# Kernel tuning notes

Measured on AMD Instinct MI355X. Metric: run time of the kernel, lower is better.

The kernel has to match this reference:

```python
import jax, jax.numpy as jnp
import numpy as np

RADIUS = 0.22
NB = 25


def fps(points, n_samples):
    """Farthest point sampling. points: [N,3] -> indices [n_samples]."""
    N = points.shape[0]

    def step(carry, _):
        mind, last = carry
        d = jnp.sum((points - points[last]) ** 2, axis=-1)  # [N]
        mind = jnp.minimum(mind, d)
        nxt = jnp.argmax(mind)
        return (mind, nxt), nxt

    init = (jnp.full((N,), jnp.inf, points.dtype), jnp.argmax(jnp.zeros((N,), points.dtype)) * 0)
    _, idxs = jax.lax.scan(step, init, None, length=n_samples - 1)
    return jnp.concatenate([jnp.zeros((1,), idxs.dtype), idxs])


def ball_knn(points, samples, radius, k):
    """For each sample, the k nearest points within `radius` (padded with the
    nearest valid neighbor, which always exists since the sample itself is in
    points with distance 0). Returns int indices [S, k]."""
    d2 = jnp.sum((samples[:, None, :] - points[None, :, :]) ** 2, axis=-1)  # [S,N]
    d2 = jnp.where(d2 <= radius * radius, d2, jnp.inf)
    neg, idx = jax.lax.top_k(-d2, k)  # ascending distance order
    valid = neg > -jnp.inf
    return jnp.where(valid, idx, idx[:, :1])


def setup_inputs() -> dict:
    key = jax.random.key(0)
    ks = jax.random.split(key, 8)
    N = 65536
    f1, f2, f3 = 80, 40, 20

    def w(k, shape):
        fan_in = shape[0]
        return jax.random.normal(k, shape, jnp.float32) * np.float32(np.sqrt(2.0 / fan_in))

    return {
        "points": jax.random.uniform(ks[0], (N, 3), jnp.float32),
        "enc_w1": w(ks[1], (3, f1)), "enc_b1": jnp.zeros((f1,), jnp.float32),
        "enc_w2": w(ks[2], (f1, f2)), "enc_b2": jnp.zeros((f2,), jnp.float32),
        "enc_w3": w(ks[3], (f2, f3)), "enc_b3": jnp.zeros((f3,), jnp.float32),
        "dec_w1": w(ks[4], (f3, f2)), "dec_b1": jnp.zeros((f2,), jnp.float32),
        "dec_w2": w(ks[5], (f2, f1)), "dec_b2": jnp.zeros((f1,), jnp.float32),
        "dec_w3": w(ks[6], (f1, NB * 3)), "dec_b3": jnp.zeros((NB * 3,), jnp.float32),
    }


def reference(points, enc_w1, enc_b1, enc_w2, enc_b2, enc_w3, enc_b3,
              dec_w1, dec_b1, dec_w2, dec_b2, dec_w3, dec_b3):
    N = points.shape[0]
    nb = dec_w3.shape[1] // 3
    n_samples = -(-N // nb)  # ceil(N * ratio), ratio = 1/nb

    # Index computations (FPS + radius query) are non-differentiable.
    p = jax.lax.stop_gradient(points)
    sample_inds = fps(p, n_samples)                    # [S]
    samples = points[sample_inds]                      # [S,3]
    rad_inds = ball_knn(p, p[sample_inds], RADIUS, nb)  # [S,nb]

    rad_cluster = jnp.repeat(jnp.arange(n_samples), nb)  # [S*nb]
    rad_points = points[rad_inds.reshape(-1)]            # [S*nb,3]
    midpoints = samples[rad_cluster]                     # [S*nb,3]
    relative = (rad_points - midpoints) / RADIUS

    # Relative autoencoder: per-point MLP -> per-cluster max pool -> decoder MLP
    h = jax.nn.relu(relative @ enc_w1 + enc_b1)
    h = jax.nn.relu(h @ enc_w2 + enc_b2)
    h = jax.nn.relu(h @ enc_w3 + enc_b3)
    feat = jnp.max(h.reshape(n_samples, nb, -1), axis=1)  # [S,f3] (mean=False)

    g = jax.nn.relu(feat @ dec_w1 + dec_b1)
    g = jax.nn.relu(g @ dec_w2 + dec_b2)
    g = g @ dec_w3 + dec_b3                              # [S, nb*3]
    relative_out = g.reshape(-1, 3)                      # [S*nb,3]

    dec_abs = relative_out * RADIUS + midpoints
    resized_deco = dec_abs.reshape(-1, nb, 3)            # [S,nb,3]
    return rad_points, rad_cluster, resized_deco
```

## Files before the change

### kernel.cpp

```cpp
#include <hip/hip_runtime.h>

typedef unsigned int u32;
typedef unsigned long long u64;

#define N_PTS 65536
#define NB_ 25
#define NSAMP 2622
#define FPS_BLOCKS 16
#define FPS_THREADS 1024
#define FPS_TOTAL (FPS_BLOCKS*FPS_THREADS)
#define PPT (N_PTS/FPS_TOTAL)
#define CAND_CAP 7900

static_assert(FPS_TOTAL*PPT == N_PTS, "fps partition");

__device__ __forceinline__ float dist2_exact(float px,float py,float pz,
                                             float qx,float qy,float qz){
  float dx=__fsub_rn(px,qx), dy=__fsub_rn(py,qy), dz=__fsub_rn(pz,qz);
  return __fadd_rn(__fadd_rn(__fmul_rn(dx,dx),__fmul_rn(dy,dy)),__fmul_rn(dz,dz));
}

__global__ void k_setup(const float* __restrict__ pts, float* __restrict__ xs,
                        float* __restrict__ ys, float* __restrict__ zs,
                        u32* __restrict__ sample_inds, u64* __restrict__ partials){
  int i = blockIdx.x*blockDim.x + threadIdx.x;
  if (i < N_PTS){ xs[i]=pts[3*i]; ys[i]=pts[3*i+1]; zs[i]=pts[3*i+2]; }
  if (blockIdx.x==0){
    if (threadIdx.x < 4*FPS_BLOCKS) partials[threadIdx.x] = 0ULL;
    if (threadIdx.x==0) sample_inds[0] = 0u;
  }
}

__global__ void __launch_bounds__(FPS_THREADS) k_fps(
    const float* __restrict__ xs, const float* __restrict__ ys,
    const float* __restrict__ zs, u32* __restrict__ sample_inds,
    u64* __restrict__ partials)
{
  __shared__ float s_q[3];
  __shared__ u64 s_wmax[FPS_THREADS/64];
  const int tid  = threadIdx.x;
  const int b    = blockIdx.x;
  const int lane = tid & 63;
  const int wv   = tid >> 6;
  const int gt   = b*FPS_THREADS + tid;

  float acc = 0.f;
  for (int j=tid; j<N_PTS; j+=FPS_THREADS) acc += xs[j]+ys[j]+zs[j];
  if (acc == -12345.678f && tid==0) sample_inds[0]=0u;

  float px[PPT],py[PPT],pz[PPT],mind[PPT];
  #pragma unroll
  for (int k=0;k<PPT;k++){
    int i = k*FPS_TOTAL + gt;
    px[k]=xs[i]; py[k]=ys[i]; pz[k]=zs[i];
    mind[k]=__builtin_huge_valf();
  }

  if (tid==0){ s_q[0]=xs[0]; s_q[1]=ys[0]; s_q[2]=zs[0]; }
  __syncthreads();

  for (int t=0; t<NSAMP-1; ++t){
    float qx=s_q[0], qy=s_q[1], qz=s_q[2];
    u64 m = 0ULL;
    #pragma unroll
    for (int k=0;k<PPT;k++){
      float d = dist2_exact(px[k],py[k],pz[k],qx,qy,qz);
      mind[k] = fminf(mind[k], d);
      u32 idx = (u32)(k*FPS_TOTAL + gt);
      u64 pk = ((u64)__float_as_uint(mind[k])<<32) | (u64)(0xFFFFFFFFu - idx);
      m = (pk>m)?pk:m;
    }
    #pragma unroll
    for (int off=1; off<64; off<<=1){ u64 o=__shfl_xor(m,off,64); if(o>m)m=o; }
    if (lane==0) s_wmax[wv]=m;
    __syncthreads();
    if (wv==0){
      u64 wm = s_wmax[lane & (FPS_THREADS/64 - 1)];
      #pragma unroll
      for (int off=1; off<16; off<<=1){ u64 o=__shfl_xor(wm,off,64); if(o>wm)wm=o; }
      if (lane==0){
        __hip_atomic_store(&partials[(t&3)*FPS_BLOCKS + b], wm,
                           __ATOMIC_RELAXED, __HIP_MEMORY_SCOPE_AGENT);
        __hip_atomic_store(&partials[((t+2)&3)*FPS_BLOCKS + b], 0ULL,
                           __ATOMIC_RELAXED, __HIP_MEMORY_SCOPE_AGENT);
      }
      u64* slot = &partials[(t&3)*FPS_BLOCKS + (lane & (FPS_BLOCKS-1))];
      u64 v;
      do { v = __hip_atomic_load(slot, __ATOMIC_RELAXED, __HIP_MEMORY_SCOPE_AGENT); }
      while (v==0ULL);
      #pragma unroll
      for (int off=1; off<16; off<<=1){ u64 o=__shfl_xor(v,off,64); if(o>v)v=o; }
      u32 widx = 0xFFFFFFFFu - (u32)(v & 0xFFFFFFFFu);
      if (lane==0){
        s_q[0]=xs[widx]; s_q[1]=ys[widx]; s_q[2]=zs[widx];
        if (b==0) sample_inds[t+1]=widx;
      }
    }
    __syncthreads();
  }
}

__global__ void __launch_bounds__(256) k_ballknn(
    const float* __restrict__ xs, const float* __restrict__ ys,
    const float* __restrict__ zs, const u32* __restrict__ sample_inds,
    u32* __restrict__ rad_inds, float* __restrict__ out_pts,
    float* __restrict__ out_cluster)
{
  __shared__ u64 s_list[CAND_CAP];
  __shared__ u64 s_red[4];
  __shared__ u64 s_win;
  __shared__ u32 s_cnt, s_first;
  const int s = blockIdx.x, tid = threadIdx.x;
  const u32 si = sample_inds[s];
  const float qx=xs[si], qy=ys[si], qz=zs[si];
  const float R2 = (float)(0.22*0.22);
  if (tid==0) s_cnt=0u;
  __syncthreads();

  for (int j=tid; j<N_PTS; j+=256){
    float d2 = dist2_exact(xs[j],ys[j],zs[j],qx,qy,qz);
    if (d2 <= R2){
      u32 pos = atomicAdd(&s_cnt,1u);
      if (pos < CAND_CAP) s_list[pos] = ((u64)__float_as_uint(d2)<<32) | (u64)j;
    }
  }
  __syncthreads();
  const int n = (int)min(s_cnt,(u32)CAND_CAP);

  for (int r=0; r<NB_; ++r){
    u64 m = ~0ULL; int mpos = -1;
    for (int p=tid; p<n; p+=256){
      u64 v=s_list[p];
      if (v<m){ m=v; mpos=p; }
    }
    u64 mm=m;
    #pragma unroll
    for (int off=1; off<64; off<<=1){ u64 o=__shfl_xor(mm,off,64); if(o<mm)mm=o; }
    if ((tid&63)==0) s_red[tid>>6]=mm;
    __syncthreads();
    if (tid==0){
      u64 w=s_red[0];
      #pragma unroll
      for (int i=1;i<4;i++) if (s_red[i]<w) w=s_red[i];
      s_win=w;
      if (r==0) s_first=(u32)(w & 0xFFFFFFFFu);
    }
    __syncthreads();
    u64 w = s_win;
    if (m==w && mpos>=0) s_list[mpos]=~0ULL;
    if (tid==0){
      u32 widx = (r < n) ? (u32)(w & 0xFFFFFFFFu) : s_first;
      int o = s*NB_ + r;
      rad_inds[o]=widx;
      out_pts[o*3+0]=xs[widx]; out_pts[o*3+1]=ys[widx]; out_pts[o*3+2]=zs[widx];
      out_cluster[o]=(float)s;
    }
    __syncthreads();
  }
}

__global__ void __launch_bounds__(256) k_mlp(
    const float* __restrict__ xs, const float* __restrict__ ys,
    const float* __restrict__ zs, const u32* __restrict__ sample_inds,
    const u32* __restrict__ rad_inds,
    const float* __restrict__ ew1, const float* __restrict__ eb1,
    const float* __restrict__ ew2, const float* __restrict__ eb2,
    const float* __restrict__ ew3, const float* __restrict__ eb3,
    const float* __restrict__ dw1, const float* __restrict__ db1,
    const float* __restrict__ dw2, const float* __restrict__ db2,
    const float* __restrict__ dw3, const float* __restrict__ db3,
    float* __restrict__ out_deco)
{
  __shared__ float rel[NB_][3], mid[3];
  __shared__ float h1[NB_][80], h2[NB_][40], h3[NB_][20];
  __shared__ float feat[20], g1[40], g2[80];
  const int s=blockIdx.x, tid=threadIdx.x;

  if (tid==0){ u32 si=sample_inds[s]; mid[0]=xs[si]; mid[1]=ys[si]; mid[2]=zs[si]; }
  __syncthreads();
  if (tid < NB_){
    u32 ri = rad_inds[s*NB_+tid];
    rel[tid][0]=(xs[ri]-mid[0])/0.22f;
    rel[tid][1]=(ys[ri]-mid[1])/0.22f;
    rel[tid][2]=(zs[ri]-mid[2])/0.22f;
  }
  __syncthreads();
  for (int o=tid;o<NB_*80;o+=256){
    int p=o/80, f=o-p*80;
    float a=eb1[f]+rel[p][0]*ew1[0*80+f]+rel[p][1]*ew1[1*80+f]+rel[p][2]*ew1[2*80+f];
    h1[p][f]=fmaxf(a,0.f);
  }
  __syncthreads();
  for (int o=tid;o<NB_*40;o+=256){
    int p=o/40, f=o-p*40;
    float a=eb2[f];
    for (int k=0;k<80;k++) a += h1[p][k]*ew2[k*40+f];
    h2[p][f]=fmaxf(a,0.f);
  }
  __syncthreads();
  for (int o=tid;o<NB_*20;o+=256){
    int p=o/20, f=o-p*20;
    float a=eb3[f];
    for (int k=0;k<40;k++) a += h2[p][k]*ew3[k*20+f];
    h3[p][f]=fmaxf(a,0.f);
  }
  __syncthreads();
  if (tid<20){
    float m=h3[0][tid];
    for (int p=1;p<NB_;p++) m=fmaxf(m,h3[p][tid]);
    feat[tid]=m;
  }
  __syncthreads();
  if (tid<40){
    float a=db1[tid];
    for (int k=0;k<20;k++) a += feat[k]*dw1[k*40+tid];
    g1[tid]=fmaxf(a,0.f);
  }
  __syncthreads();
  if (tid<80){
    float a=db2[tid];
    for (int k=0;k<40;k++) a += g1[k]*dw2[k*80+tid];
    g2[tid]=fmaxf(a,0.f);
  }
  __syncthreads();
  if (tid<NB_*3){
    float a=db3[tid];
    for (int k=0;k<80;k++) a += g2[k]*dw3[k*75+tid];
    int p=tid/3, c=tid-p*3;
    out_deco[(s*NB_+p)*3+c] = a*0.22f + mid[c];
  }
}

extern "C" void kernel_launch(void* const* d_in, const int* in_sizes, int n_in,
                              void* d_out, int out_size, void* d_ws, size_t ws_size,
                              hipStream_t stream){
  const float* pts=(const float*)d_in[0];
  const float* ew1=(const float*)d_in[1];  const float* eb1=(const float*)d_in[2];
  const float* ew2=(const float*)d_in[3];  const float* eb2=(const float*)d_in[4];
  const float* ew3=(const float*)d_in[5];  const float* eb3=(const float*)d_in[6];
  const float* dw1=(const float*)d_in[7];  const float* db1=(const float*)d_in[8];
  const float* dw2=(const float*)d_in[9];  const float* db2=(const float*)d_in[10];
  const float* dw3=(const float*)d_in[11]; const float* db3=(const float*)d_in[12];

  float* out = (float*)d_out;
  float* out_pts     = out;
  float* out_cluster = out + NSAMP*NB_*3;
  float* out_deco    = out + NSAMP*NB_*4;

  char* ws = (char*)d_ws;
  float* xs = (float*)ws;
  float* ys = xs + N_PTS;
  float* zs = ys + N_PTS;
  u32* sinds    = (u32*)(zs + N_PTS);
  u64* partials = (u64*)(sinds + 4096);
  u32* rinds    = (u32*)(partials + 4*FPS_BLOCKS);

  k_setup<<<(N_PTS+255)/256, 256, 0, stream>>>(pts, xs, ys, zs, sinds, partials);
  k_fps<<<FPS_BLOCKS, FPS_THREADS, 0, stream>>>(xs, ys, zs, sinds, partials);
  k_ballknn<<<NSAMP, 256, 0, stream>>>(xs, ys, zs, sinds, rinds, out_pts, out_cluster);
  k_mlp<<<NSAMP, 256, 0, stream>>>(xs, ys, zs, sinds, rinds,
                                   ew1,eb1,ew2,eb2,ew3,eb3,
                                   dw1,db1,dw2,db2,dw3,db3, out_deco);
}
```

Before: 5.873 ms.

## Restructure FPS as 128 single-wave blocks with tagged global ring exchange

Replaces the 16×1024-thread FPS kernel, which needed intra-block syncthreads and a two-level reduction, with 128 single-wavefront blocks. Each wave publishes its local argmax key and the winning point's coordinates into a phase-indexed global ring, with iteration tags packed into the keys. Every wave then polls all 128 slots and reduces redundantly, so no separate broadcast step or barrier is needed. The cost is wider polling traffic per iteration, a 16-bit index packing that only holds for N ≤ 65536, and coordinate splitting across two words. It also drops the dummy warm-up loop over all points.

```diff
diff --git a/kernel.cpp b/kernel.cpp
--- a/kernel.cpp
+++ b/kernel.cpp
@@ -6,13 +6,13 @@
 #define N_PTS 65536
 #define NB_ 25
 #define NSAMP 2622
-#define FPS_BLOCKS 16
-#define FPS_THREADS 1024
-#define FPS_TOTAL (FPS_BLOCKS*FPS_THREADS)
-#define PPT (N_PTS/FPS_TOTAL)
+#define FPSW 128
+#define PPW 8
+#define STRIDE (FPSW*64)
+#define RING_U64 (4*FPSW + 4*FPSW*2)
 #define CAND_CAP 7900
 
-static_assert(FPS_TOTAL*PPT == N_PTS, "fps partition");
+static_assert(STRIDE*PPW == N_PTS, "fps partition");
 
 __device__ __forceinline__ float dist2_exact(float px,float py,float pz,
                                              float qx,float qy,float qz){
@@ -20,83 +20,102 @@
   return __fadd_rn(__fadd_rn(__fmul_rn(dx,dx),__fmul_rn(dy,dy)),__fmul_rn(dz,dz));
 }
 
+__device__ __forceinline__ u64 ald(const u64* p){
+  return __hip_atomic_load(p, __ATOMIC_RELAXED, __HIP_MEMORY_SCOPE_AGENT);
+}
+__device__ __forceinline__ void ast(u64* p, u64 v){
+  __hip_atomic_store(p, v, __ATOMIC_RELAXED, __HIP_MEMORY_SCOPE_AGENT);
+}
+
 __global__ void k_setup(const float* __restrict__ pts, float* __restrict__ xs,
                         float* __restrict__ ys, float* __restrict__ zs,
-                        u32* __restrict__ sample_inds, u64* __restrict__ partials){
+                        u32* __restrict__ sample_inds, u64* __restrict__ ring){
   int i = blockIdx.x*blockDim.x + threadIdx.x;
   if (i < N_PTS){ xs[i]=pts[3*i]; ys[i]=pts[3*i+1]; zs[i]=pts[3*i+2]; }
   if (blockIdx.x==0){
-    if (threadIdx.x < 4*FPS_BLOCKS) partials[threadIdx.x] = 0ULL;
+    for (int j=threadIdx.x; j<RING_U64; j+=256) ring[j]=0ULL;
     if (threadIdx.x==0) sample_inds[0] = 0u;
   }
 }
 
-__global__ void __launch_bounds__(FPS_THREADS) k_fps(
+__global__ void __launch_bounds__(64) k_fps(
     const float* __restrict__ xs, const float* __restrict__ ys,
-    const float* __restrict__ zs, u32* __restrict__ sample_inds,
-    u64* __restrict__ partials)
+    const float* __restrict__ zs, u32* __restrict__ sinds,
+    u64* __restrict__ ring)
 {
-  __shared__ float s_q[3];
-  __shared__ u64 s_wmax[FPS_THREADS/64];
-  const int tid  = threadIdx.x;
-  const int b    = blockIdx.x;
-  const int lane = tid & 63;
-  const int wv   = tid >> 6;
-  const int gt   = b*FPS_THREADS + tid;
-
-  float acc = 0.f;
-  for (int j=tid; j<N_PTS; j+=FPS_THREADS) acc += xs[j]+ys[j]+zs[j];
-  if (acc == -12345.678f && tid==0) sample_inds[0]=0u;
-
-  float px[PPT],py[PPT],pz[PPT],mind[PPT];
-  #pragma unroll
-  for (int k=0;k<PPT;k++){
-    int i = k*FPS_TOTAL + gt;
+  u64* keys = ring;
+  u64* cs   = ring + 4*FPSW;
+  const int w = blockIdx.x, lane = threadIdx.x;
+  const int gt = w*64 + lane;
+
+  float px[PPW],py[PPW],pz[PPW],mind[PPW];
+#pragma unroll
+  for (int k=0;k<PPW;k++){
+    int i = k*STRIDE + gt;
     px[k]=xs[i]; py[k]=ys[i]; pz[k]=zs[i];
     mind[k]=__builtin_huge_valf();
   }
-
-  if (tid==0){ s_q[0]=xs[0]; s_q[1]=ys[0]; s_q[2]=zs[0]; }
-  __syncthreads();
+  float qx=xs[0], qy=ys[0], qz=zs[0];
 
   for (int t=0; t<NSAMP-1; ++t){
-    float qx=s_q[0], qy=s_q[1], qz=s_q[2];
-    u64 m = 0ULL;
-    #pragma unroll
-    for (int k=0;k<PPT;k++){
+    const u64 tag = (u64)((t+1) & 0xFFFF);
+    u64 bk = 0ULL;
+#pragma unroll
+    for (int k=0;k<PPW;k++){
       float d = dist2_exact(px[k],py[k],pz[k],qx,qy,qz);
       mind[k] = fminf(mind[k], d);
-      u32 idx = (u32)(k*FPS_TOTAL + gt);
-      u64 pk = ((u64)__float_as_uint(mind[k])<<32) | (u64)(0xFFFFFFFFu - idx);
-      m = (pk>m)?pk:m;
-    }
-    #pragma unroll
-    for (int off=1; off<64; off<<=1){ u64 o=__shfl_xor(m,off,64); if(o>m)m=o; }
-    if (lane==0) s_wmax[wv]=m;
-    __syncthreads();
-    if (wv==0){
-      u64 wm = s_wmax[lane & (FPS_THREADS/64 - 1)];
-      #pragma unroll
-      for (int off=1; off<16; off<<=1){ u64 o=__shfl_xor(wm,off,64); if(o>wm)wm=o; }
-      if (lane==0){
-        __hip_atomic_store(&partials[(t&3)*FPS_BLOCKS + b], wm,
-                           __ATOMIC_RELAXED, __HIP_MEMORY_SCOPE_AGENT);
-        __hip_atomic_store(&partials[((t+2)&3)*FPS_BLOCKS + b], 0ULL,
-                           __ATOMIC_RELAXED, __HIP_MEMORY_SCOPE_AGENT);
-      }
-      u64* slot = &partials[(t&3)*FPS_BLOCKS + (lane & (FPS_BLOCKS-1))];
-      u64 v;
-      do { v = __hip_atomic_load(slot, __ATOMIC_RELAXED, __HIP_MEMORY_SCOPE_AGENT); }
-      while (v==0ULL);
-      #pragma unroll
-      for (int off=1; off<16; off<<=1){ u64 o=__shfl_xor(v,off,64); if(o>v)v=o; }
-      u32 widx = 0xFFFFFFFFu - (u32)(v & 0xFFFFFFFFu);
-      if (lane==0){
-        s_q[0]=xs[widx]; s_q[1]=ys[widx]; s_q[2]=zs[widx];
-        if (b==0) sample_inds[t+1]=widx;
-      }
-    }
-    __syncthreads();
+      u64 pk = ((u64)__float_as_uint(mind[k])<<32)
+             | ((u64)(0xFFFFu - (u32)(k*STRIDE+gt))<<16) | tag;
+      bk = (pk>bk)?pk:bk;
+    }
+    u64 wk = bk;
+#pragma unroll
+    for (int off=1; off<64; off<<=1){ u64 o=__shfl_xor(wk,off,64); if(o>wk)wk=o; }
+
+    const int ph = t & 3;
+    if (bk == wk){
+      u32 cidx = 0xFFFFu - (u32)((wk>>16)&0xFFFFu);
+      float cx=0.f, cy=0.f, cz=0.f;
+#pragma unroll
+      for (int k=0;k<PPW;k++) if (cidx == (u32)(k*STRIDE+gt)){ cx=px[k]; cy=py[k]; cz=pz[k]; }
+      u32 zb = __float_as_uint(cz);
+      u64 c0 = ((u64)__float_as_uint(cx)<<32) | ((u64)(zb & 0xFFFFu)<<16) | (u64)cidx;
+      u64 c1 = ((u64)__float_as_uint(cy)<<32) | ((u64)(zb >> 16   )<<16) | (u64)cidx;
+      ast(&cs[(ph*FPSW+w)*2],   c0);
+      ast(&cs[(ph*FPSW+w)*2+1], c1);
+      ast(&keys[ph*FPSW+w], wk);
+    }
+
+    const u64* kp = keys + ph*FPSW;
+    const u64* cp = cs   + ph*FPSW*2;
+    u64 kl,kh,c0a,c1a,c0b,c1b;
+    for(;;){
+      kl  = ald(kp + lane);        kh  = ald(kp + 64 + lane);
+      c0a = ald(cp + 2*lane);      c1a = ald(cp + 2*lane + 1);
+      c0b = ald(cp + 2*(64+lane)); c1b = ald(cp + 2*(64+lane) + 1);
+      if (__all(((kl&0xFFFFull)==tag) && ((kh&0xFFFFull)==tag))) break;
+    }
+
+    bool hi = kh > kl;
+    u64 kb = hi ? kh : kl;
+    u64 W = kb;
+#pragma unroll
+    for (int off=1; off<64; off<<=1){ u64 o=__shfl_xor(W,off,64); if(o>W)W=o; }
+    u32 widx = 0xFFFFu - (u32)((W>>16)&0xFFFFu);
+    u64 sc0 = hi?c0b:c0a, sc1 = hi?c1b:c1a;
+    int myslot = lane + (hi?64:0);
+    u64 mb = __ballot(kb == W);
+    int src = __ffsll(mb) - 1;
+    u64 c0w = __shfl(sc0, src, 64);
+    u64 c1w = __shfl(sc1, src, 64);
+    int slotw = __shfl(myslot, src, 64);
+    while ( (u32)(c0w&0xFFFFu)!=widx || (u32)(c1w&0xFFFFu)!=widx ){
+      c0w = ald(cp + 2*slotw); c1w = ald(cp + 2*slotw + 1);
+    }
+    qx = __uint_as_float((u32)(c0w>>32));
+    qy = __uint_as_float((u32)(c1w>>32));
+    qz = __uint_as_float( (u32)((c0w>>16)&0xFFFFu) | ((u32)((c1w>>16)&0xFFFFu)<<16) );
+    if (gt==0) sinds[t+1] = widx;
   }
 }
 
@@ -251,12 +270,12 @@
   float* xs = (float*)ws;
   float* ys = xs + N_PTS;
   float* zs = ys + N_PTS;
-  u32* sinds    = (u32*)(zs + N_PTS);
-  u64* partials = (u64*)(sinds + 4096);
-  u32* rinds    = (u32*)(partials + 4*FPS_BLOCKS);
-
-  k_setup<<<(N_PTS+255)/256, 256, 0, stream>>>(pts, xs, ys, zs, sinds, partials);
-  k_fps<<<FPS_BLOCKS, FPS_THREADS, 0, stream>>>(xs, ys, zs, sinds, partials);
+  u32* sinds = (u32*)(zs + N_PTS);
+  u64* ring  = (u64*)(sinds + 4096);
+  u32* rinds = (u32*)(ring + RING_U64);
+
+  k_setup<<<(N_PTS+255)/256, 256, 0, stream>>>(pts, xs, ys, zs, sinds, ring);
+  k_fps<<<FPSW, 64, 0, stream>>>(xs, ys, zs, sinds, ring);
   k_ballknn<<<NSAMP, 256, 0, stream>>>(xs, ys, zs, sinds, rinds, out_pts, out_cluster);
   k_mlp<<<NSAMP, 256, 0, stream>>>(xs, ys, zs, sinds, rinds,
                                    ew1,eb1,ew2,eb2,ew3,eb3,
```

Result: slower. 9.056 ms (+54.2%).

## Replace brute-force FPS with grid-cell pruned single-block FPS

Applied to the files above, without the earlier changes.

Farthest point sampling now bins points into a 10x10x10 grid with per-cell bounding boxes, sorted into a compact float4 array. Each iteration updates only cells whose box lower bound to the new sample is below that cell's current max min-distance, and keeps a per-cell max key. This replaces the 16-block cross-block spin-wait reduction with one 1024-thread block, removing global synchronization and most distance work. It adds histogram, prefix and scatter kernels, and leaves the serial loop on a single CU with irregular per-cell work. Tie-breaking relies on a 16-bit packed index that only holds for N=65536.

```diff
diff --git a/kernel.cpp b/kernel.cpp
--- a/kernel.cpp
+++ b/kernel.cpp
@@ -6,13 +6,8 @@
 #define N_PTS 65536
 #define NB_ 25
 #define NSAMP 2622
-#define FPS_BLOCKS 16
-#define FPS_THREADS 1024
-#define FPS_TOTAL (FPS_BLOCKS*FPS_THREADS)
-#define PPT (N_PTS/FPS_TOTAL)
+#define NCELL 1000
 #define CAND_CAP 7900
-
-static_assert(FPS_TOTAL*PPT == N_PTS, "fps partition");
 
 __device__ __forceinline__ float dist2_exact(float px,float py,float pz,
                                              float qx,float qy,float qz){
@@ -22,78 +17,145 @@
 
 __global__ void k_setup(const float* __restrict__ pts, float* __restrict__ xs,
                         float* __restrict__ ys, float* __restrict__ zs,
-                        u32* __restrict__ sample_inds, u64* __restrict__ partials){
+                        u32* __restrict__ sinds, u32* __restrict__ cnt,
+                        u32* __restrict__ fill, u32* __restrict__ amin,
+                        u32* __restrict__ amax){
   int i = blockIdx.x*blockDim.x + threadIdx.x;
   if (i < N_PTS){ xs[i]=pts[3*i]; ys[i]=pts[3*i+1]; zs[i]=pts[3*i+2]; }
-  if (blockIdx.x==0){
-    if (threadIdx.x < 4*FPS_BLOCKS) partials[threadIdx.x] = 0ULL;
-    if (threadIdx.x==0) sample_inds[0] = 0u;
-  }
-}
-
-__global__ void __launch_bounds__(FPS_THREADS) k_fps(
+  if (i < 1024){
+    cnt[i]=0u; fill[i]=0u;
+    amin[i]=0x7F800000u; amin[1024+i]=0x7F800000u; amin[2048+i]=0x7F800000u;
+    amax[i]=0u;          amax[1024+i]=0u;          amax[2048+i]=0u;
+  }
+  if (i==0) sinds[0]=0u;
+}
+
+__device__ __forceinline__ int cell_of(float x,float y,float z){
+  int ix = min(9,(int)(x*10.0f)), iy = min(9,(int)(y*10.0f)), iz = min(9,(int)(z*10.0f));
+  return ix + 10*iy + 100*iz;
+}
+
+__global__ void k_hist(const float* __restrict__ xs, const float* __restrict__ ys,
+                       const float* __restrict__ zs, u32* __restrict__ cnt,
+                       u32* __restrict__ amin, u32* __restrict__ amax){
+  int i = blockIdx.x*blockDim.x + threadIdx.x;
+  if (i >= N_PTS) return;
+  float x=xs[i], y=ys[i], z=zs[i];
+  int c = cell_of(x,y,z);
+  atomicAdd(&cnt[c],1u);
+  atomicMin(&amin[c],      __float_as_uint(x)); atomicMax(&amax[c],      __float_as_uint(x));
+  atomicMin(&amin[1024+c], __float_as_uint(y)); atomicMax(&amax[1024+c], __float_as_uint(y));
+  atomicMin(&amin[2048+c], __float_as_uint(z)); atomicMax(&amax[2048+c], __float_as_uint(z));
+}
+
+__global__ void __launch_bounds__(1024) k_prefix(const u32* __restrict__ cnt,
+                                                 u32* __restrict__ base){
+  __shared__ u32 s[1024];
+  int tid = threadIdx.x;
+  u32 x = (tid < NCELL) ? cnt[tid] : 0u;
+  s[tid] = x; __syncthreads();
+  for (int off=1; off<1024; off<<=1){
+    u32 v = (tid >= off) ? s[tid-off] : 0u;
+    __syncthreads();
+    s[tid] += v;
+    __syncthreads();
+  }
+  if (tid < NCELL) base[tid] = s[tid] - x;
+}
+
+__global__ void k_scatter(const float* __restrict__ xs, const float* __restrict__ ys,
+                          const float* __restrict__ zs, const u32* __restrict__ base,
+                          u32* __restrict__ fill, float4* __restrict__ P4,
+                          u32* __restrict__ OID){
+  int i = blockIdx.x*blockDim.x + threadIdx.x;
+  if (i >= N_PTS) return;
+  float x=xs[i], y=ys[i], z=zs[i];
+  int c = cell_of(x,y,z);
+  u32 pos = base[c] + atomicAdd(&fill[c],1u);
+  P4[pos] = make_float4(x,y,z,__builtin_huge_valf());
+  OID[pos] = (u32)i;
+}
+
+__global__ void __launch_bounds__(1024) k_fps1(
     const float* __restrict__ xs, const float* __restrict__ ys,
-    const float* __restrict__ zs, u32* __restrict__ sample_inds,
-    u64* __restrict__ partials)
+    const float* __restrict__ zs, const u32* __restrict__ g_cnt,
+    const u32* __restrict__ g_base, const u32* __restrict__ g_amin,
+    const u32* __restrict__ g_amax, float4* __restrict__ P4,
+    const u32* __restrict__ OID, u32* __restrict__ sinds)
 {
+  __shared__ float s_lox[NCELL], s_hix[NCELL], s_loy[NCELL], s_hiy[NCELL],
+                   s_loz[NCELL], s_hiz[NCELL];
+  __shared__ u32 s_cnt[NCELL], s_base[NCELL];
+  __shared__ u64 s_ckey[NCELL];
+  __shared__ u64 s_red[16];
   __shared__ float s_q[3];
-  __shared__ u64 s_wmax[FPS_THREADS/64];
-  const int tid  = threadIdx.x;
-  const int b    = blockIdx.x;
-  const int lane = tid & 63;
-  const int wv   = tid >> 6;
-  const int gt   = b*FPS_THREADS + tid;
-
-  float acc = 0.f;
-  for (int j=tid; j<N_PTS; j+=FPS_THREADS) acc += xs[j]+ys[j]+zs[j];
-  if (acc == -12345.678f && tid==0) sample_inds[0]=0u;
-
-  float px[PPT],py[PPT],pz[PPT],mind[PPT];
-  #pragma unroll
-  for (int k=0;k<PPT;k++){
-    int i = k*FPS_TOTAL + gt;
-    px[k]=xs[i]; py[k]=ys[i]; pz[k]=zs[i];
-    mind[k]=__builtin_huge_valf();
-  }
-
+
+  const int tid = threadIdx.x;
+  const int lane = tid & 63, w = tid >> 6;
+
+  for (int i = tid; i < NCELL; i += 1024){
+    u32 c0 = g_cnt[i];
+    s_cnt[i]=c0; s_base[i]=g_base[i];
+    s_lox[i]=__uint_as_float(g_amin[i]);      s_hix[i]=__uint_as_float(g_amax[i]);
+    s_loy[i]=__uint_as_float(g_amin[1024+i]); s_hiy[i]=__uint_as_float(g_amax[1024+i]);
+    s_loz[i]=__uint_as_float(g_amin[2048+i]); s_hiz[i]=__uint_as_float(g_amax[2048+i]);
+    s_ckey[i] = c0 ? 0x7F80000000000000ULL : 0ULL;
+  }
   if (tid==0){ s_q[0]=xs[0]; s_q[1]=ys[0]; s_q[2]=zs[0]; }
   __syncthreads();
 
   for (int t=0; t<NSAMP-1; ++t){
-    float qx=s_q[0], qy=s_q[1], qz=s_q[2];
-    u64 m = 0ULL;
+    const float qx=s_q[0], qy=s_q[1], qz=s_q[2];
+
+    const int c = (lane<<4) | w;
+    bool need = false;
+    if (c < NCELL && s_cnt[c]){
+      float ub = __uint_as_float((u32)(s_ckey[c]>>32));
+      float dx = fmaxf(fmaxf(__fsub_rn(s_lox[c],qx), __fsub_rn(qx,s_hix[c])), 0.f);
+      float dy = fmaxf(fmaxf(__fsub_rn(s_loy[c],qy), __fsub_rn(qy,s_hiy[c])), 0.f);
+      float dz = fmaxf(fmaxf(__fsub_rn(s_loz[c],qz), __fsub_rn(qz,s_hiz[c])), 0.f);
+      float lb = __fadd_rn(__fadd_rn(__fmul_rn(dx,dx),__fmul_rn(dy,dy)),__fmul_rn(dz,dz));
+      need = lb < ub;
+    }
+
+    u64 todo = __ballot(need);
+    while (todo){
+      int l = __ffsll((unsigned long long)todo) - 1;
+      todo &= todo - 1;
+      int sc = (l<<4) | w;
+      u32 base = s_base[sc], cn = s_cnt[sc];
+      u64 mykey = 0ULL;
+      for (u32 j = (u32)lane; j < cn; j += 64u){
+        float4 v = P4[base + j];
+        float d2 = dist2_exact(v.x,v.y,v.z,qx,qy,qz);
+        float nm = fminf(v.w, d2);
+        if (nm < v.w) ((float*)(P4 + base + j))[3] = nm;
+        u32 oid = OID[base + j];
+        u64 kk = ((u64)__float_as_uint(nm)<<32)
+               | ((u64)(oid ^ 0xFFFFu)<<16) | (u64)(base + j);
+        if (kk > mykey) mykey = kk;
+      }
+      #pragma unroll
+      for (int off=1; off<64; off<<=1){ u64 o=__shfl_xor(mykey,off,64); if(o>mykey)mykey=o; }
+      if (lane==0) s_ckey[sc] = mykey;
+    }
+    __syncthreads();
+
+    u64 kk = (tid < NCELL) ? s_ckey[tid] : 0ULL;
     #pragma unroll
-    for (int k=0;k<PPT;k++){
-      float d = dist2_exact(px[k],py[k],pz[k],qx,qy,qz);
-      mind[k] = fminf(mind[k], d);
-      u32 idx = (u32)(k*FPS_TOTAL + gt);
-      u64 pk = ((u64)__float_as_uint(mind[k])<<32) | (u64)(0xFFFFFFFFu - idx);
-      m = (pk>m)?pk:m;
-    }
-    #pragma unroll
-    for (int off=1; off<64; off<<=1){ u64 o=__shfl_xor(m,off,64); if(o>m)m=o; }
-    if (lane==0) s_wmax[wv]=m;
-    __syncthreads();
-    if (wv==0){
-      u64 wm = s_wmax[lane & (FPS_THREADS/64 - 1)];
+    for (int off=1; off<64; off<<=1){ u64 o=__shfl_xor(kk,off,64); if(o>kk)kk=o; }
+    if (lane==0) s_red[w]=kk;
+    __syncthreads();
+    if (w==0){
+      u64 r = (lane<16) ? s_red[lane] : 0ULL;
       #pragma unroll
-      for (int off=1; off<16; off<<=1){ u64 o=__shfl_xor(wm,off,64); if(o>wm)wm=o; }
+      for (int off=1; off<16; off<<=1){ u64 o=__shfl_xor(r,off,64); if(o>r)r=o; }
       if (lane==0){
-        __hip_atomic_store(&partials[(t&3)*FPS_BLOCKS + b], wm,
-                           __ATOMIC_RELAXED, __HIP_MEMORY_SCOPE_AGENT);
-        __hip_atomic_store(&partials[((t+2)&3)*FPS_BLOCKS + b], 0ULL,
-                           __ATOMIC_RELAXED, __HIP_MEMORY_SCOPE_AGENT);
-      }
-      u64* slot = &partials[(t&3)*FPS_BLOCKS + (lane & (FPS_BLOCKS-1))];
-      u64 v;
-      do { v = __hip_atomic_load(slot, __ATOMIC_RELAXED, __HIP_MEMORY_SCOPE_AGENT); }
-      while (v==0ULL);
-      #pragma unroll
-      for (int off=1; off<16; off<<=1){ u64 o=__shfl_xor(v,off,64); if(o>v)v=o; }
-      u32 widx = 0xFFFFFFFFu - (u32)(v & 0xFFFFFFFFu);
-      if (lane==0){
-        s_q[0]=xs[widx]; s_q[1]=ys[widx]; s_q[2]=zs[widx];
-        if (b==0) sample_inds[t+1]=widx;
+        u32 spos = (u32)(r & 0xFFFFu);
+        u32 widx = (((u32)(r>>16)) & 0xFFFFu) ^ 0xFFFFu;
+        float4 wp = P4[spos];
+        s_q[0]=wp.x; s_q[1]=wp.y; s_q[2]=wp.z;
+        sinds[t+1]=widx;
       }
     }
     __syncthreads();
@@ -248,17 +310,26 @@
   float* out_deco    = out + NSAMP*NB_*4;
 
   char* ws = (char*)d_ws;
-  float* xs = (float*)ws;
-  float* ys = xs + N_PTS;
-  float* zs = ys + N_PTS;
-  u32* sinds    = (u32*)(zs + N_PTS);
-  u64* partials = (u64*)(sinds + 4096);
-  u32* rinds    = (u32*)(partials + 4*FPS_BLOCKS);
-
-  k_setup<<<(N_PTS+255)/256, 256, 0, stream>>>(pts, xs, ys, zs, sinds, partials);
-  k_fps<<<FPS_BLOCKS, FPS_THREADS, 0, stream>>>(xs, ys, zs, sinds, partials);
+  float* xs   = (float*)ws;
+  float* ys   = xs + N_PTS;
+  float* zs   = ys + N_PTS;
+  u32* sinds  = (u32*)(zs + N_PTS);
+  u32* rinds  = sinds + 4096;
+  u32* cnt    = rinds + 65552;
+  u32* fill   = cnt + 1024;
+  u32* cbase  = fill + 1024;
+  u32* amin   = cbase + 1024;
+  u32* amax   = amin + 3*1024;
+  u32* OID    = amax + 3*1024;
+  float4* P4  = (float4*)(OID + N_PTS);
+
+  k_setup  <<<(N_PTS+255)/256, 256, 0, stream>>>(pts, xs, ys, zs, sinds, cnt, fill, amin, amax);
+  k_hist   <<<(N_PTS+255)/256, 256, 0, stream>>>(xs, ys, zs, cnt, amin, amax);
+  k_prefix <<<1, 1024, 0, stream>>>(cnt, cbase);
+  k_scatter<<<(N_PTS+255)/256, 256, 0, stream>>>(xs, ys, zs, cbase, fill, P4, OID);
+  k_fps1   <<<1, 1024, 0, stream>>>(xs, ys, zs, cnt, cbase, amin, amax, P4, OID, sinds);
   k_ballknn<<<NSAMP, 256, 0, stream>>>(xs, ys, zs, sinds, rinds, out_pts, out_cluster);
-  k_mlp<<<NSAMP, 256, 0, stream>>>(xs, ys, zs, sinds, rinds,
-                                   ew1,eb1,ew2,eb2,ew3,eb3,
-                                   dw1,db1,dw2,db2,dw3,db3, out_deco);
-}
+  k_mlp    <<<NSAMP, 256, 0, stream>>>(xs, ys, zs, sinds, rinds,
+                                       ew1,eb1,ew2,eb2,ew3,eb3,
+                                       dw1,db1,dw2,db2,dw3,db3, out_deco);
+}
```

Result: slower. 11.98 ms (+104.0%).
